# Kernel optimization log

Measured on AMD Instinct MI355X. Metric: run time of the kernel, lower is better.

## Reference

```python
import jax, jax.numpy as jnp
import numpy as np

N_NODES = 8192
N_EDGES = 262144
D_FEAT = 512
NHID = 32
LATENT = 16


def setup_inputs() -> dict:
    key = jax.random.key(0)
    ks = jax.random.split(key, 12)
    inp = {
        "features": jax.random.normal(ks[0], (N_NODES, D_FEAT), dtype=jnp.float32),
        "edge_src": jax.random.randint(ks[1], (N_EDGES,), 0, N_NODES, dtype=jnp.int32),
        "edge_dst": jax.random.randint(ks[2], (N_EDGES,), 0, N_NODES, dtype=jnp.int32),
        "edge_weight": jax.random.uniform(ks[3], (N_EDGES,), dtype=jnp.float32),
        # GCEncoder params (GCNConv: out = A @ (x W) + b)
        "Wg1": jax.random.normal(ks[4], (D_FEAT, NHID), dtype=jnp.float32) / np.sqrt(D_FEAT),
        "bg1": jnp.zeros((NHID,), jnp.float32),
        "Wg2": jax.random.normal(ks[5], (NHID, LATENT), dtype=jnp.float32) / np.sqrt(NHID),
        "bg2": jnp.zeros((LATENT,), jnp.float32),
        # MLP encoder params
        "We1": jax.random.normal(ks[6], (D_FEAT, NHID), dtype=jnp.float32) / np.sqrt(D_FEAT),
        "be1": jnp.zeros((NHID,), jnp.float32),
        "We2": jax.random.normal(ks[7], (NHID, LATENT), dtype=jnp.float32) / np.sqrt(NHID),
        "be2": jnp.zeros((LATENT,), jnp.float32),
        # MLP decoder params (latent -> features)
        "Wd1": jax.random.normal(ks[8], (LATENT, NHID), dtype=jnp.float32) / np.sqrt(LATENT),
        "bd1": jnp.zeros((NHID,), jnp.float32),
        "Wd2": jax.random.normal(ks[9], (NHID, D_FEAT), dtype=jnp.float32) / np.sqrt(NHID),
        "bd2": jnp.zeros((D_FEAT,), jnp.float32),
    }
    return inp


def _gcn_conv(x, W, b, edge_src, edge_dst, edge_weight, n_nodes):
    # transform then sparse aggregate: A @ (x W) + b
    xw = x @ W                                   # [N, out]
    msg = xw[edge_src] * edge_weight[:, None]    # [E, out]
    agg = jax.ops.segment_sum(msg, edge_dst, num_segments=n_nodes)
    return agg + b


def reference(features, edge_src, edge_dst, edge_weight,
              Wg1, bg1, Wg2, bg2, We1, be1, We2, be2, Wd1, bd1, Wd2, bd2):
    n = features.shape[0]
    # GCEncoder (dropout p=0.0)
    h = jax.nn.relu(_gcn_conv(features, Wg1, bg1, edge_src, edge_dst, edge_weight, n))
    za = jax.nn.relu(_gcn_conv(h, Wg2, bg2, edge_src, edge_dst, edge_weight, n))
    # MLP encoder
    zx = jax.nn.relu(jax.nn.relu(features @ We1 + be1) @ We2 + be2)
    # concat latents
    z = jnp.concatenate([za, zx], axis=1)        # [N, 2*latent]
    # inner-product decoder: sigmoid(z z^T)  -> [N, N]
    adj_recon = jax.nn.sigmoid(z @ z.T)
    # feature decoder MLP
    feat_recon = jax.nn.relu(jax.nn.relu(zx @ Wd1 + bd1) @ Wd2 + bd2)
    return adj_recon, feat_recon, z
```

## Files before the change

kernel.cpp:

```cpp
#include <hip/hip_runtime.h>

typedef unsigned short ushort_t;
typedef __attribute__((ext_vector_type(8))) short short8;
typedef __attribute__((ext_vector_type(4))) float floatx4;
typedef __attribute__((ext_vector_type(2))) float floatx2;

#define N_NODES 8192
#define N_EDGES 262144
#define D_FEAT 512
#define NHID 32
#define LATENT 16

#define ADJ_OFF 0
#define FEAT_OFF (8192*8192)
#define Z_OFF (8192*8192 + 8192*512)

static __device__ __forceinline__ ushort_t f2bf(float f) {
    unsigned int u = __float_as_uint(f);
    unsigned int r = u + 0x7fffu + ((u >> 16) & 1u);
    return (ushort_t)(r >> 16);
}

__global__ __launch_bounds__(256) void k_zero(int* __restrict__ counts) {
    int i = blockIdx.x * 256 + threadIdx.x;
    if (i < N_NODES) counts[i] = 0;
}

__global__ __launch_bounds__(256) void k_hist(const int* __restrict__ edst, int* __restrict__ counts) {
    int e = blockIdx.x * 256 + threadIdx.x;
    atomicAdd(&counts[edst[e]], 1);
}

__global__ __launch_bounds__(1024) void k_scan(const int* __restrict__ counts,
                                               int* __restrict__ offs, int* __restrict__ cursor) {
    __shared__ int sdata[1024];
    int t = threadIdx.x;
    int base = t * 8;
    int c[8], local[8];
    int s = 0;
    #pragma unroll
    for (int j = 0; j < 8; j++) { c[j] = counts[base + j]; }
    #pragma unroll
    for (int j = 0; j < 8; j++) { local[j] = s; s += c[j]; }
    sdata[t] = s;
    __syncthreads();
    for (int off = 1; off < 1024; off <<= 1) {
        int v = sdata[t];
        int add = (t >= off) ? sdata[t - off] : 0;
        __syncthreads();
        sdata[t] = v + add;
        __syncthreads();
    }
    int excl = (t == 0) ? 0 : sdata[t - 1];
    #pragma unroll
    for (int j = 0; j < 8; j++) {
        int o = excl + local[j];
        offs[base + j] = o;
        cursor[base + j] = o;
    }
}

__global__ __launch_bounds__(256) void k_scatter(const int* __restrict__ esrc,
                                                 const int* __restrict__ edst,
                                                 const float* __restrict__ ew,
                                                 int* __restrict__ cursor,
                                                 int2* __restrict__ sedge) {
    int e = blockIdx.x * 256 + threadIdx.x;
    int d = edst[e];
    int pos = atomicAdd(&cursor[d], 1);
    sedge[pos] = make_int2(esrc[e], __float_as_int(ew[e]));
}

__global__ __launch_bounds__(256) void k_enc(const float* __restrict__ feat,
                                             const float* __restrict__ Wg1,
                                             const float* __restrict__ We1,
                                             const float* __restrict__ be1,
                                             const float* __restrict__ We2,
                                             const float* __restrict__ be2,
                                             float* __restrict__ xwg,
                                             float* __restrict__ zxf) {
    __shared__ float WL[32][64];
    __shared__ float FL[32][33];
    __shared__ float HE[32][33];
    int tid = threadIdx.x;
    int cr = tid & 15;
    int nr = tid >> 4;
    int m0 = blockIdx.x * 32;
    float acc[2][4] = {};

    for (int kt = 0; kt < 16; kt++) {
        __syncthreads();
        {
            int i = tid;
            #pragma unroll
            for (int j = 0; j < 8; j++, i += 256) {
                int k = i >> 6, c = i & 63;
                int kg = kt * 32 + k;
                WL[k][c] = (c < 32) ? Wg1[kg * 32 + c] : We1[kg * 32 + (c - 32)];
            }
        }
        {
            int n = tid >> 3, q = tid & 7;
            float4 v = *(const float4*)(feat + (m0 + n) * 512 + kt * 32 + q * 4);
            FL[n][q * 4 + 0] = v.x; FL[n][q * 4 + 1] = v.y;
            FL[n][q * 4 + 2] = v.z; FL[n][q * 4 + 3] = v.w;
        }
        __syncthreads();
        #pragma unroll 4
        for (int k = 0; k < 32; k++) {
            float4 w = *(const float4*)&WL[k][cr * 4];
            float f0 = FL[nr * 2 + 0][k];
            float f1 = FL[nr * 2 + 1][k];
            acc[0][0] += f0 * w.x; acc[0][1] += f0 * w.y;
            acc[0][2] += f0 * w.z; acc[0][3] += f0 * w.w;
            acc[1][0] += f1 * w.x; acc[1][1] += f1 * w.y;
            acc[1][2] += f1 * w.z; acc[1][3] += f1 * w.w;
        }
    }
    int cg = cr * 4;
    if (cg < 32) {
        #pragma unroll
        for (int j = 0; j < 2; j++) {
            float4 v = make_float4(acc[j][0], acc[j][1], acc[j][2], acc[j][3]);
            *(float4*)(xwg + (m0 + nr * 2 + j) * 32 + cg) = v;
        }
    } else {
        int hc = cg - 32;
        #pragma unroll
        for (int j = 0; j < 2; j++) {
            #pragma unroll
            for (int t = 0; t < 4; t++) {
                float v = acc[j][t] + be1[hc + t];
                HE[nr * 2 + j][hc + t] = v > 0.f ? v : 0.f;
            }
        }
    }
    __syncthreads();
    int n = tid >> 3, j0 = (tid & 7) * 2;
    float s0 = be2[j0], s1 = be2[j0 + 1];
    #pragma unroll 8
    for (int cc = 0; cc < 32; cc++) {
        float h = HE[n][cc];
        s0 += h * We2[cc * 16 + j0];
        s1 += h * We2[cc * 16 + j0 + 1];
    }
    s0 = s0 > 0.f ? s0 : 0.f;
    s1 = s1 > 0.f ? s1 : 0.f;
    *(float2*)(zxf + (m0 + n) * 16 + j0) = make_float2(s0, s1);
}

__global__ __launch_bounds__(256) void k_agg1(const float* __restrict__ xwg,
                                              const int* __restrict__ offs,
                                              const int* __restrict__ counts,
                                              const int2* __restrict__ sedge,
                                              const float* __restrict__ bg1,
                                              const float* __restrict__ Wg2,
                                              float* __restrict__ hw2) {
    __shared__ float hsh[8][33];
    int ln = threadIdx.x >> 5, c = threadIdx.x & 31;
    int n = blockIdx.x * 8 + ln;
    int st = offs[n], en = st + counts[n];
    float acc = 0.f;
    int i = st;
    for (; i + 4 <= en; i += 4) {
        int2 e0 = sedge[i], e1 = sedge[i + 1], e2 = sedge[i + 2], e3 = sedge[i + 3];
        float s0 = __int_as_float(e0.y) * xwg[e0.x * 32 + c];
        float s1 = __int_as_float(e1.y) * xwg[e1.x * 32 + c];
        float s2 = __int_as_float(e2.y) * xwg[e2.x * 32 + c];
        float s3 = __int_as_float(e3.y) * xwg[e3.x * 32 + c];
        acc += (s0 + s1) + (s2 + s3);
    }
    for (; i < en; i++) {
        int2 e = sedge[i];
        acc += __int_as_float(e.y) * xwg[e.x * 32 + c];
    }
    float h = acc + bg1[c];
    hsh[ln][c] = h > 0.f ? h : 0.f;
    __syncthreads();
    if (threadIdx.x < 128) {
        int l2 = threadIdx.x >> 4, j = threadIdx.x & 15;
        float s2 = 0.f;
        #pragma unroll 8
        for (int cc = 0; cc < 32; cc++) s2 += hsh[l2][cc] * Wg2[cc * 16 + j];
        hw2[(blockIdx.x * 8 + l2) * 16 + j] = s2;
    }
}

__global__ __launch_bounds__(256) void k_agg2(const float* __restrict__ hw2,
                                              const int* __restrict__ offs,
                                              const int* __restrict__ counts,
                                              const int2* __restrict__ sedge,
                                              const float* __restrict__ bg2,
                                              const float* __restrict__ zxf,
                                              ushort_t* __restrict__ zbf,
                                              float* __restrict__ zout) {
    int ln = threadIdx.x >> 4, c = threadIdx.x & 15;
    int n = blockIdx.x * 16 + ln;
    int st = offs[n], en = st + counts[n];
    float acc = 0.f;
    int i = st;
    for (; i + 4 <= en; i += 4) {
        int2 e0 = sedge[i], e1 = sedge[i + 1], e2 = sedge[i + 2], e3 = sedge[i + 3];
        float s0 = __int_as_float(e0.y) * hw2[e0.x * 16 + c];
        float s1 = __int_as_float(e1.y) * hw2[e1.x * 16 + c];
        float s2 = __int_as_float(e2.y) * hw2[e2.x * 16 + c];
        float s3 = __int_as_float(e3.y) * hw2[e3.x * 16 + c];
        acc += (s0 + s1) + (s2 + s3);
    }
    for (; i < en; i++) {
        int2 e = sedge[i];
        acc += __int_as_float(e.y) * hw2[e.x * 16 + c];
    }
    float za = acc + bg2[c];
    za = za > 0.f ? za : 0.f;
    float zx = zxf[n * 16 + c];
    zout[n * 32 + c] = za;
    zout[n * 32 + 16 + c] = zx;
    zbf[n * 32 + c] = f2bf(za);
    zbf[n * 32 + 16 + c] = f2bf(zx);
}

__global__ __launch_bounds__(256) void k_feat(const float* __restrict__ zxf,
                                              const float* __restrict__ Wd1,
                                              const float* __restrict__ bd1,
                                              const float* __restrict__ Wd2,
                                              const float* __restrict__ bd2,
                                              float* __restrict__ outF) {
    __shared__ float ZL[16][17];
    __shared__ float HT[16][33];
    int tid = threadIdx.x;
    int m0 = blockIdx.x * 16;
    {
        int n = tid >> 4, k = tid & 15;
        ZL[n][k] = zxf[(m0 + n) * 16 + k];
    }
    __syncthreads();
    {
        int o = tid * 2;
        int n = o >> 5, c = o & 31;
        float s0 = bd1[c], s1 = bd1[c + 1];
        #pragma unroll
        for (int k = 0; k < 16; k++) {
            float z = ZL[n][k];
            s0 += z * Wd1[k * 32 + c];
            s1 += z * Wd1[k * 32 + c + 1];
        }
        HT[n][c] = s0 > 0.f ? s0 : 0.f;
        HT[n][c + 1] = s1 > 0.f ? s1 : 0.f;
    }
    __syncthreads();
    int c2 = tid * 2;
    floatx2 acc[16];
    #pragma unroll
    for (int n = 0; n < 16; n++) acc[n] = (floatx2){0.f, 0.f};
    for (int k = 0; k < 32; k++) {
        float2 w = *(const float2*)(Wd2 + k * 512 + c2);
        #pragma unroll
        for (int n = 0; n < 16; n++) {
            float t = HT[n][k];
            acc[n].x += t * w.x;
            acc[n].y += t * w.y;
        }
    }
    float b0 = bd2[c2], b1 = bd2[c2 + 1];
    #pragma unroll
    for (int n = 0; n < 16; n++) {
        float s0 = acc[n].x + b0, s1 = acc[n].y + b1;
        s0 = s0 > 0.f ? s0 : 0.f;
        s1 = s1 > 0.f ? s1 : 0.f;
        floatx2 pk = {s0, s1};
        __builtin_nontemporal_store(pk, (floatx2*)(outF + (size_t)(m0 + n) * 512 + c2));
    }
}

__global__ __launch_bounds__(256) void k_adj(const ushort_t* __restrict__ zbf,
                                             float* __restrict__ out) {
    int l = threadIdx.x & 63;
    int wv = threadIdx.x >> 6;
    int strip = blockIdx.x & 15;
    int rt = (blockIdx.x >> 4) * 4 + wv;
    int q = l >> 4, cl = l & 15;
    int m0 = rt * 16, c0 = strip * 512;
    short8 a = *(const short8*)(zbf + (m0 + cl) * 32 + q * 8);
    for (int g = 0; g < 8; g++) {
        int cb = c0 + g * 64;
        short8 b0 = *(const short8*)(zbf + (cb + 4 * cl + 0) * 32 + q * 8);
        short8 b1 = *(const short8*)(zbf + (cb + 4 * cl + 1) * 32 + q * 8);
        short8 b2 = *(const short8*)(zbf + (cb + 4 * cl + 2) * 32 + q * 8);
        short8 b3 = *(const short8*)(zbf + (cb + 4 * cl + 3) * 32 + q * 8);
        floatx4 zv = {0, 0, 0, 0};
        floatx4 a0 = __builtin_amdgcn_mfma_f32_16x16x32_bf16(a, b0, zv, 0, 0, 0);
        floatx4 a1 = __builtin_amdgcn_mfma_f32_16x16x32_bf16(a, b1, zv, 0, 0, 0);
        floatx4 a2 = __builtin_amdgcn_mfma_f32_16x16x32_bf16(a, b2, zv, 0, 0, 0);
        floatx4 a3 = __builtin_amdgcn_mfma_f32_16x16x32_bf16(a, b3, zv, 0, 0, 0);
        #pragma unroll
        for (int r = 0; r < 4; r++) {
            floatx4 v;
            v.x = 1.f / (1.f + __expf(-a0[r]));
            v.y = 1.f / (1.f + __expf(-a1[r]));
            v.z = 1.f / (1.f + __expf(-a2[r]));
            v.w = 1.f / (1.f + __expf(-a3[r]));
            int row = m0 + q * 4 + r;
            __builtin_nontemporal_store(v, (floatx4*)(out + (size_t)row * 8192 + cb + 4 * cl));
        }
    }
}

extern "C" void kernel_launch(void* const* d_in, const int* in_sizes, int n_in,
                              void* d_out, int out_size, void* d_ws, size_t ws_size,
                              hipStream_t stream) {
    const float* feat = (const float*)d_in[0];
    const int* esrc = (const int*)d_in[1];
    const int* edst = (const int*)d_in[2];
    const float* ew = (const float*)d_in[3];
    const float* Wg1 = (const float*)d_in[4];
    const float* bg1 = (const float*)d_in[5];
    const float* Wg2 = (const float*)d_in[6];
    const float* bg2 = (const float*)d_in[7];
    const float* We1 = (const float*)d_in[8];
    const float* be1 = (const float*)d_in[9];
    const float* We2 = (const float*)d_in[10];
    const float* be2 = (const float*)d_in[11];
    const float* Wd1 = (const float*)d_in[12];
    const float* bd1 = (const float*)d_in[13];
    const float* Wd2 = (const float*)d_in[14];
    const float* bd2 = (const float*)d_in[15];
    float* out = (float*)d_out;

    char* ws = (char*)d_ws;
    float* xwg      = (float*)(ws + 0);
    float* zxf      = (float*)(ws + 1048576);
    float* hw2      = (float*)(ws + 1572864);
    ushort_t* zbf   = (ushort_t*)(ws + 2097152);
    int* counts     = (int*)(ws + 2621440);
    int* offs       = (int*)(ws + 2654208);
    int* cursor     = (int*)(ws + 2686976);
    int2* sedge     = (int2*)(ws + 2719744);

    k_zero<<<32, 256, 0, stream>>>(counts);
    k_hist<<<N_EDGES / 256, 256, 0, stream>>>(edst, counts);
    k_scan<<<1, 1024, 0, stream>>>(counts, offs, cursor);
    k_scatter<<<N_EDGES / 256, 256, 0, stream>>>(esrc, edst, ew, cursor, sedge);
    k_enc<<<N_NODES / 32, 256, 0, stream>>>(feat, Wg1, We1, be1, We2, be2, xwg, zxf);
    k_agg1<<<N_NODES / 8, 256, 0, stream>>>(xwg, offs, counts, sedge, bg1, Wg2, hw2);
    k_agg2<<<N_NODES / 16, 256, 0, stream>>>(hw2, offs, counts, sedge, bg2, zxf,
                                             zbf, out + Z_OFF);
    k_feat<<<N_NODES / 16, 256, 0, stream>>>(zxf, Wd1, bd1, Wd2, bd2, out + FEAT_OFF);
    k_adj<<<(N_NODES / 16 / 4) * 16, 256, 0, stream>>>(zbf, out + ADJ_OFF);
}
```

Baseline: 454.7 us.

## Fuse graph build and GCN aggregation into persistent kernel with grid barriers

```diff
diff --git a/kernel.cpp b/kernel.cpp
--- a/kernel.cpp
+++ b/kernel.cpp
@@ -15,60 +15,25 @@
 #define FEAT_OFF (8192*8192)
 #define Z_OFF (8192*8192 + 8192*512)
 
+#define GCN_BLOCKS 512
+
 static __device__ __forceinline__ ushort_t f2bf(float f) {
     unsigned int u = __float_as_uint(f);
     unsigned int r = u + 0x7fffu + ((u >> 16) & 1u);
     return (ushort_t)(r >> 16);
 }
 
-__global__ __launch_bounds__(256) void k_zero(int* __restrict__ counts) {
-    int i = blockIdx.x * 256 + threadIdx.x;
-    if (i < N_NODES) counts[i] = 0;
-}
-
-__global__ __launch_bounds__(256) void k_hist(const int* __restrict__ edst, int* __restrict__ counts) {
-    int e = blockIdx.x * 256 + threadIdx.x;
-    atomicAdd(&counts[edst[e]], 1);
-}
-
-__global__ __launch_bounds__(1024) void k_scan(const int* __restrict__ counts,
-                                               int* __restrict__ offs, int* __restrict__ cursor) {
-    __shared__ int sdata[1024];
-    int t = threadIdx.x;
-    int base = t * 8;
-    int c[8], local[8];
-    int s = 0;
-    #pragma unroll
-    for (int j = 0; j < 8; j++) { c[j] = counts[base + j]; }
-    #pragma unroll
-    for (int j = 0; j < 8; j++) { local[j] = s; s += c[j]; }
-    sdata[t] = s;
+static __device__ __forceinline__ void gbar(int* bar, int target) {
+    __threadfence();
     __syncthreads();
-    for (int off = 1; off < 1024; off <<= 1) {
-        int v = sdata[t];
-        int add = (t >= off) ? sdata[t - off] : 0;
-        __syncthreads();
-        sdata[t] = v + add;
-        __syncthreads();
-    }
-    int excl = (t == 0) ? 0 : sdata[t - 1];
-    #pragma unroll
-    for (int j = 0; j < 8; j++) {
-        int o = excl + local[j];
-        offs[base + j] = o;
-        cursor[base + j] = o;
-    }
-}
-
-__global__ __launch_bounds__(256) void k_scatter(const int* __restrict__ esrc,
-                                                 const int* __restrict__ edst,
-                                                 const float* __restrict__ ew,
-                                                 int* __restrict__ cursor,
-                                                 int2* __restrict__ sedge) {
-    int e = blockIdx.x * 256 + threadIdx.x;
-    int d = edst[e];
-    int pos = atomicAdd(&cursor[d], 1);
-    sedge[pos] = make_int2(esrc[e], __float_as_int(ew[e]));
+    if (threadIdx.x == 0) {
+        __hip_atomic_fetch_add(bar, 1, __ATOMIC_ACQ_REL, __HIP_MEMORY_SCOPE_AGENT);
+        while (__hip_atomic_load(bar, __ATOMIC_ACQUIRE, __HIP_MEMORY_SCOPE_AGENT) < target) {
+            __builtin_amdgcn_s_sleep(8);
+        }
+    }
+    __syncthreads();
+    __threadfence();
 }
 
 __global__ __launch_bounds__(256) void k_enc(const float* __restrict__ feat,
@@ -78,11 +43,17 @@
                                              const float* __restrict__ We2,
                                              const float* __restrict__ be2,
                                              float* __restrict__ xwg,
-                                             float* __restrict__ zxf) {
+                                             float* __restrict__ zxf,
+                                             int* __restrict__ counts,
+                                             int* __restrict__ bar) {
     __shared__ float WL[32][64];
     __shared__ float FL[32][33];
     __shared__ float HE[32][33];
     int tid = threadIdx.x;
+    int gid = blockIdx.x * 256 + tid;
+    if (gid < N_NODES) counts[gid] = 0;
+    if (gid == 0) *bar = 0;
+
     int cr = tid & 15;
     int nr = tid >> 4;
     int m0 = blockIdx.x * 32;
@@ -149,159 +120,212 @@
     *(float2*)(zxf + (m0 + n) * 16 + j0) = make_float2(s0, s1);
 }
 
-__global__ __launch_bounds__(256) void k_agg1(const float* __restrict__ xwg,
-                                              const int* __restrict__ offs,
-                                              const int* __restrict__ counts,
-                                              const int2* __restrict__ sedge,
-                                              const float* __restrict__ bg1,
-                                              const float* __restrict__ Wg2,
-                                              float* __restrict__ hw2) {
-    __shared__ float hsh[8][33];
-    int ln = threadIdx.x >> 5, c = threadIdx.x & 31;
-    int n = blockIdx.x * 8 + ln;
-    int st = offs[n], en = st + counts[n];
-    float acc = 0.f;
-    int i = st;
-    for (; i + 4 <= en; i += 4) {
-        int2 e0 = sedge[i], e1 = sedge[i + 1], e2 = sedge[i + 2], e3 = sedge[i + 3];
-        float s0 = __int_as_float(e0.y) * xwg[e0.x * 32 + c];
-        float s1 = __int_as_float(e1.y) * xwg[e1.x * 32 + c];
-        float s2 = __int_as_float(e2.y) * xwg[e2.x * 32 + c];
-        float s3 = __int_as_float(e3.y) * xwg[e3.x * 32 + c];
-        acc += (s0 + s1) + (s2 + s3);
-    }
-    for (; i < en; i++) {
-        int2 e = sedge[i];
-        acc += __int_as_float(e.y) * xwg[e.x * 32 + c];
-    }
-    float h = acc + bg1[c];
-    hsh[ln][c] = h > 0.f ? h : 0.f;
-    __syncthreads();
-    if (threadIdx.x < 128) {
-        int l2 = threadIdx.x >> 4, j = threadIdx.x & 15;
+__global__ __launch_bounds__(256, 2) void k_gcn(const int* __restrict__ esrc,
+                                                const int* __restrict__ edst,
+                                                const float* __restrict__ ew,
+                                                const float* __restrict__ xwg,
+                                                const float* __restrict__ bg1,
+                                                const float* __restrict__ Wg2,
+                                                const float* __restrict__ bg2,
+                                                const float* __restrict__ zxf,
+                                                int* __restrict__ counts,
+                                                int* __restrict__ offs,
+                                                int* __restrict__ cursor,
+                                                int2* __restrict__ sedge,
+                                                float* __restrict__ hw2,
+                                                ushort_t* __restrict__ zbf,
+                                                float* __restrict__ zout,
+                                                int* __restrict__ bar) {
+    __shared__ int ps[256];
+    __shared__ float hsh[16][33];
+    int tid = threadIdx.x;
+    int b = blockIdx.x;
+
+    int e0 = b * 512;
+    #pragma unroll
+    for (int r = 0; r < 2; r++) {
+        int e = e0 + r * 256 + tid;
+        atomicAdd(&counts[edst[e]], 1);
+    }
+    gbar(bar, GCN_BLOCKS);
+
+    if (b == 0) {
+        int base = tid * 32;
+        int loc[32];
+        int s = 0;
+        #pragma unroll
+        for (int j = 0; j < 32; j++) { loc[j] = s; s += counts[base + j]; }
+        ps[tid] = s;
+        __syncthreads();
+        for (int off = 1; off < 256; off <<= 1) {
+            int v = ps[tid];
+            int a = (tid >= off) ? ps[tid - off] : 0;
+            __syncthreads();
+            ps[tid] = v + a;
+            __syncthreads();
+        }
+        int excl = tid ? ps[tid - 1] : 0;
+        #pragma unroll
+        for (int j = 0; j < 32; j++) {
+            int o = excl + loc[j];
+            offs[base + j] = o;
+            cursor[base + j] = o;
+        }
+    }
+    gbar(bar, 2 * GCN_BLOCKS);
+
+    #pragma unroll
+    for (int r = 0; r < 2; r++) {
+        int e = e0 + r * 256 + tid;
+        int d = edst[e];
+        int pos = atomicAdd(&cursor[d], 1);
+        sedge[pos] = make_int2(esrc[e], __float_as_int(ew[e]));
+    }
+    gbar(bar, 3 * GCN_BLOCKS);
+
+    {
+        int ln = tid >> 5, c = tid & 31;
+        for (int pass = 0; pass < 2; pass++) {
+            int n = b * 16 + pass * 8 + ln;
+            int st = offs[n], en = st + counts[n];
+            float acc = 0.f;
+            int i = st;
+            for (; i + 4 <= en; i += 4) {
+                int2 q0 = sedge[i], q1 = sedge[i + 1], q2 = sedge[i + 2], q3 = sedge[i + 3];
+                float v0 = __int_as_float(q0.y) * xwg[q0.x * 32 + c];
+                float v1 = __int_as_float(q1.y) * xwg[q1.x * 32 + c];
+                float v2 = __int_as_float(q2.y) * xwg[q2.x * 32 + c];
+                float v3 = __int_as_float(q3.y) * xwg[q3.x * 32 + c];
+                acc += (v0 + v1) + (v2 + v3);
+            }
+            for (; i < en; i++) {
+                int2 q = sedge[i];
+                acc += __int_as_float(q.y) * xwg[q.x * 32 + c];
+            }
+            float h = acc + bg1[c];
+            hsh[pass * 8 + ln][c] = h > 0.f ? h : 0.f;
+        }
+        __syncthreads();
+        int n2 = tid >> 4, j = tid & 15;
         float s2 = 0.f;
         #pragma unroll 8
-        for (int cc = 0; cc < 32; cc++) s2 += hsh[l2][cc] * Wg2[cc * 16 + j];
-        hw2[(blockIdx.x * 8 + l2) * 16 + j] = s2;
-    }
-}
-
-__global__ __launch_bounds__(256) void k_agg2(const float* __restrict__ hw2,
-                                              const int* __restrict__ offs,
-                                              const int* __restrict__ counts,
-                                              const int2* __restrict__ sedge,
-                                              const float* __restrict__ bg2,
-                                              const float* __restrict__ zxf,
-                                              ushort_t* __restrict__ zbf,
-                                              float* __restrict__ zout) {
-    int ln = threadIdx.x >> 4, c = threadIdx.x & 15;
-    int n = blockIdx.x * 16 + ln;
-    int st = offs[n], en = st + counts[n];
-    float acc = 0.f;
-    int i = st;
-    for (; i + 4 <= en; i += 4) {
-        int2 e0 = sedge[i], e1 = sedge[i + 1], e2 = sedge[i + 2], e3 = sedge[i + 3];
-        float s0 = __int_as_float(e0.y) * hw2[e0.x * 16 + c];
-        float s1 = __int_as_float(e1.y) * hw2[e1.x * 16 + c];
-        float s2 = __int_as_float(e2.y) * hw2[e2.x * 16 + c];
-        float s3 = __int_as_float(e3.y) * hw2[e3.x * 16 + c];
-        acc += (s0 + s1) + (s2 + s3);
-    }
-    for (; i < en; i++) {
-        int2 e = sedge[i];
-        acc += __int_as_float(e.y) * hw2[e.x * 16 + c];
-    }
-    float za = acc + bg2[c];
-    za = za > 0.f ? za : 0.f;
-    float zx = zxf[n * 16 + c];
-    zout[n * 32 + c] = za;
-    zout[n * 32 + 16 + c] = zx;
-    zbf[n * 32 + c] = f2bf(za);
-    zbf[n * 32 + 16 + c] = f2bf(zx);
-}
-
-__global__ __launch_bounds__(256) void k_feat(const float* __restrict__ zxf,
-                                              const float* __restrict__ Wd1,
-                                              const float* __restrict__ bd1,
-                                              const float* __restrict__ Wd2,
-                                              const float* __restrict__ bd2,
-                                              float* __restrict__ outF) {
+        for (int cc = 0; cc < 32; cc++) s2 += hsh[n2][cc] * Wg2[cc * 16 + j];
+        hw2[(b * 16 + n2) * 16 + j] = s2;
+    }
+    gbar(bar, 4 * GCN_BLOCKS);
+
+    {
+        int ln = tid >> 4, c = tid & 15;
+        int n = b * 16 + ln;
+        int st = offs[n], en = st + counts[n];
+        float acc = 0.f;
+        int i = st;
+        for (; i + 4 <= en; i += 4) {
+            int2 q0 = sedge[i], q1 = sedge[i + 1], q2 = sedge[i + 2], q3 = sedge[i + 3];
+            float v0 = __int_as_float(q0.y) * hw2[q0.x * 16 + c];
+            float v1 = __int_as_float(q1.y) * hw2[q1.x * 16 + c];
+            float v2 = __int_as_float(q2.y) * hw2[q2.x * 16 + c];
+            float v3 = __int_as_float(q3.y) * hw2[q3.x * 16 + c];
+            acc += (v0 + v1) + (v2 + v3);
+        }
+        for (; i < en; i++) {
+            int2 q = sedge[i];
+            acc += __int_as_float(q.y) * hw2[q.x * 16 + c];
+        }
+        float za = acc + bg2[c];
+        za = za > 0.f ? za : 0.f;
+        float zx = zxf[n * 16 + c];
+        zout[n * 32 + c] = za;
+        zout[n * 32 + 16 + c] = zx;
+        zbf[n * 32 + c] = f2bf(za);
+        zbf[n * 32 + 16 + c] = f2bf(zx);
+    }
+}
+
+__global__ __launch_bounds__(256) void k_out(const ushort_t* __restrict__ zbf,
+                                             const float* __restrict__ zxf,
+                                             const float* __restrict__ Wd1,
+                                             const float* __restrict__ bd1,
+                                             const float* __restrict__ Wd2,
+                                             const float* __restrict__ bd2,
+                                             float* __restrict__ out) {
     __shared__ float ZL[16][17];
     __shared__ float HT[16][33];
     int tid = threadIdx.x;
-    int m0 = blockIdx.x * 16;
-    {
-        int n = tid >> 4, k = tid & 15;
-        ZL[n][k] = zxf[(m0 + n) * 16 + k];
-    }
-    __syncthreads();
-    {
-        int o = tid * 2;
-        int n = o >> 5, c = o & 31;
-        float s0 = bd1[c], s1 = bd1[c + 1];
-        #pragma unroll
-        for (int k = 0; k < 16; k++) {
-            float z = ZL[n][k];
-            s0 += z * Wd1[k * 32 + c];
-            s1 += z * Wd1[k * 32 + c + 1];
-        }
-        HT[n][c] = s0 > 0.f ? s0 : 0.f;
-        HT[n][c + 1] = s1 > 0.f ? s1 : 0.f;
-    }
-    __syncthreads();
-    int c2 = tid * 2;
-    floatx2 acc[16];
-    #pragma unroll
-    for (int n = 0; n < 16; n++) acc[n] = (floatx2){0.f, 0.f};
-    for (int k = 0; k < 32; k++) {
-        float2 w = *(const float2*)(Wd2 + k * 512 + c2);
+    if (blockIdx.x < 2048) {
+        float* adj = out + ADJ_OFF;
+        int l = tid & 63;
+        int wv = tid >> 6;
+        int strip = blockIdx.x & 15;
+        int rt = (blockIdx.x >> 4) * 4 + wv;
+        int q = l >> 4, cl = l & 15;
+        int m0 = rt * 16, c0 = strip * 512;
+        short8 a = *(const short8*)(zbf + (m0 + cl) * 32 + q * 8);
+        for (int g = 0; g < 8; g++) {
+            int cb = c0 + g * 64;
+            short8 b0 = *(const short8*)(zbf + (cb + 4 * cl + 0) * 32 + q * 8);
+            short8 b1 = *(const short8*)(zbf + (cb + 4 * cl + 1) * 32 + q * 8);
+            short8 b2 = *(const short8*)(zbf + (cb + 4 * cl + 2) * 32 + q * 8);
+            short8 b3 = *(const short8*)(zbf + (cb + 4 * cl + 3) * 32 + q * 8);
+            floatx4 zv = {0, 0, 0, 0};
+            floatx4 a0 = __builtin_amdgcn_mfma_f32_16x16x32_bf16(a, b0, zv, 0, 0, 0);
+            floatx4 a1 = __builtin_amdgcn_mfma_f32_16x16x32_bf16(a, b1, zv, 0, 0, 0);
+            floatx4 a2 = __builtin_amdgcn_mfma_f32_16x16x32_bf16(a, b2, zv, 0, 0, 0);
+            floatx4 a3 = __builtin_amdgcn_mfma_f32_16x16x32_bf16(a, b3, zv, 0, 0, 0);
+            #pragma unroll
+            for (int r = 0; r < 4; r++) {
+                floatx4 v;
+                v.x = 1.f / (1.f + __expf(-a0[r]));
+                v.y = 1.f / (1.f + __expf(-a1[r]));
+                v.z = 1.f / (1.f + __expf(-a2[r]));
+                v.w = 1.f / (1.f + __expf(-a3[r]));
+                int row = m0 + q * 4 + r;
+                __builtin_nontemporal_store(v, (floatx4*)(adj + (size_t)row * 8192 + cb + 4 * cl));
+            }
+        }
+    } else {
+        float* outF = out + FEAT_OFF;
+        int m0 = (blockIdx.x - 2048) * 16;
+        {
+            int n = tid >> 4, k = tid & 15;
+            ZL[n][k] = zxf[(m0 + n) * 16 + k];
+        }
+        __syncthreads();
+        {
+            int o = tid * 2;
+            int n = o >> 5, c = o & 31;
+            float s0 = bd1[c], s1 = bd1[c + 1];
+            #pragma unroll
+            for (int k = 0; k < 16; k++) {
+                float z = ZL[n][k];
+                s0 += z * Wd1[k * 32 + c];
+                s1 += z * Wd1[k * 32 + c + 1];
+            }
+            HT[n][c] = s0 > 0.f ? s0 : 0.f;
+            HT[n][c + 1] = s1 > 0.f ? s1 : 0.f;
+        }
+        __syncthreads();
+        int c2 = tid * 2;
+        floatx2 acc[16];
+        #pragma unroll
+        for (int n = 0; n < 16; n++) acc[n] = (floatx2){0.f, 0.f};
+        for (int k = 0; k < 32; k++) {
+            float2 w = *(const float2*)(Wd2 + k * 512 + c2);
+            #pragma unroll
+            for (int n = 0; n < 16; n++) {
+                float t = HT[n][k];
+                acc[n].x += t * w.x;
+                acc[n].y += t * w.y;
+            }
+        }
+        float b0 = bd2[c2], b1 = bd2[c2 + 1];
         #pragma unroll
         for (int n = 0; n < 16; n++) {
-            float t = HT[n][k];
-            acc[n].x += t * w.x;
-            acc[n].y += t * w.y;
-        }
-    }
-    float b0 = bd2[c2], b1 = bd2[c2 + 1];
-    #pragma unroll
-    for (int n = 0; n < 16; n++) {
-        float s0 = acc[n].x + b0, s1 = acc[n].y + b1;
-        s0 = s0 > 0.f ? s0 : 0.f;
-        s1 = s1 > 0.f ? s1 : 0.f;
-        floatx2 pk = {s0, s1};
-        __builtin_nontemporal_store(pk, (floatx2*)(outF + (size_t)(m0 + n) * 512 + c2));
-    }
-}
-
-__global__ __launch_bounds__(256) void k_adj(const ushort_t* __restrict__ zbf,
-                                             float* __restrict__ out) {
-    int l = threadIdx.x & 63;
-    int wv = threadIdx.x >> 6;
-    int strip = blockIdx.x & 15;
-    int rt = (blockIdx.x >> 4) * 4 + wv;
-    int q = l >> 4, cl = l & 15;
-    int m0 = rt * 16, c0 = strip * 512;
-    short8 a = *(const short8*)(zbf + (m0 + cl) * 32 + q * 8);
-    for (int g = 0; g < 8; g++) {
-        int cb = c0 + g * 64;
-        short8 b0 = *(const short8*)(zbf + (cb + 4 * cl + 0) * 32 + q * 8);
-        short8 b1 = *(const short8*)(zbf + (cb + 4 * cl + 1) * 32 + q * 8);
-        short8 b2 = *(const short8*)(zbf + (cb + 4 * cl + 2) * 32 + q * 8);
-        short8 b3 = *(const short8*)(zbf + (cb + 4 * cl + 3) * 32 + q * 8);
-        floatx4 zv = {0, 0, 0, 0};
-        floatx4 a0 = __builtin_amdgcn_mfma_f32_16x16x32_bf16(a, b0, zv, 0, 0, 0);
-        floatx4 a1 = __builtin_amdgcn_mfma_f32_16x16x32_bf16(a, b1, zv, 0, 0, 0);
-        floatx4 a2 = __builtin_amdgcn_mfma_f32_16x16x32_bf16(a, b2, zv, 0, 0, 0);
-        floatx4 a3 = __builtin_amdgcn_mfma_f32_16x16x32_bf16(a, b3, zv, 0, 0, 0);
-        #pragma unroll
-        for (int r = 0; r < 4; r++) {
-            floatx4 v;
-            v.x = 1.f / (1.f + __expf(-a0[r]));
-            v.y = 1.f / (1.f + __expf(-a1[r]));
-            v.z = 1.f / (1.f + __expf(-a2[r]));
-            v.w = 1.f / (1.f + __expf(-a3[r]));
-            int row = m0 + q * 4 + r;
-            __builtin_nontemporal_store(v, (floatx4*)(out + (size_t)row * 8192 + cb + 4 * cl));
+            float s0 = acc[n].x + b0, s1 = acc[n].y + b1;
+            s0 = s0 > 0.f ? s0 : 0.f;
+            s1 = s1 > 0.f ? s1 : 0.f;
+            floatx2 pk = {s0, s1};
+            __builtin_nontemporal_store(pk, (floatx2*)(outF + (size_t)(m0 + n) * 512 + c2));
         }
     }
 }
@@ -335,16 +359,13 @@
     int* counts     = (int*)(ws + 2621440);
     int* offs       = (int*)(ws + 2654208);
     int* cursor     = (int*)(ws + 2686976);
-    int2* sedge     = (int2*)(ws + 2719744);
-
-    k_zero<<<32, 256, 0, stream>>>(counts);
-    k_hist<<<N_EDGES / 256, 256, 0, stream>>>(edst, counts);
-    k_scan<<<1, 1024, 0, stream>>>(counts, offs, cursor);
-    k_scatter<<<N_EDGES / 256, 256, 0, stream>>>(esrc, edst, ew, cursor, sedge);
-    k_enc<<<N_NODES / 32, 256, 0, stream>>>(feat, Wg1, We1, be1, We2, be2, xwg, zxf);
-    k_agg1<<<N_NODES / 8, 256, 0, stream>>>(xwg, offs, counts, sedge, bg1, Wg2, hw2);
-    k_agg2<<<N_NODES / 16, 256, 0, stream>>>(hw2, offs, counts, sedge, bg2, zxf,
-                                             zbf, out + Z_OFF);
-    k_feat<<<N_NODES / 16, 256, 0, stream>>>(zxf, Wd1, bd1, Wd2, bd2, out + FEAT_OFF);
-    k_adj<<<(N_NODES / 16 / 4) * 16, 256, 0, stream>>>(zbf, out + ADJ_OFF);
-}
+    int* bar        = (int*)(ws + 2719744);
+    int2* sedge     = (int2*)(ws + 2719872);
+
+    k_enc<<<N_NODES / 32, 256, 0, stream>>>(feat, Wg1, We1, be1, We2, be2,
+                                            xwg, zxf, counts, bar);
+    k_gcn<<<GCN_BLOCKS, 256, 0, stream>>>(esrc, edst, ew, xwg, bg1, Wg2, bg2, zxf,
+                                          counts, offs, cursor, sedge, hw2,
+                                          zbf, out + Z_OFF, bar);
+    k_out<<<2048 + 512, 256, 0, stream>>>(zbf, zxf, Wd1, bd1, Wd2, bd2, out);
+}
```

Result: slower. 865.6 us (+90.4%).

## Fuse zeroing into encoder, merge feature and adjacency decoders, use fast sigmoid

Applied to the files above, without the earlier changes.

```diff
diff --git a/kernel.cpp b/kernel.cpp
--- a/kernel.cpp
+++ b/kernel.cpp
@@ -21,9 +21,78 @@
     return (ushort_t)(r >> 16);
 }
 
-__global__ __launch_bounds__(256) void k_zero(int* __restrict__ counts) {
-    int i = blockIdx.x * 256 + threadIdx.x;
-    if (i < N_NODES) counts[i] = 0;
+static __device__ __forceinline__ float fsig(float x) {
+    float e = __builtin_amdgcn_exp2f(x * -1.44269504f);
+    return __builtin_amdgcn_rcpf(1.f + e);
+}
+
+__global__ __launch_bounds__(256) void k_enc(const float* __restrict__ feat,
+                                             const float* __restrict__ Wg1,
+                                             const float* __restrict__ We1,
+                                             const float* __restrict__ be1,
+                                             const float* __restrict__ We2,
+                                             const float* __restrict__ be2,
+                                             float* __restrict__ xwg,
+                                             float* __restrict__ zxf,
+                                             int* __restrict__ counts) {
+    __shared__ float WL[32][64];
+    __shared__ float FL[16][36];
+    __shared__ float HE[16][33];
+    int tid = threadIdx.x;
+    int gid = blockIdx.x * 256 + tid;
+    if (gid < N_NODES) counts[gid] = 0;
+
+    int n = tid >> 4;
+    int cr = tid & 15;
+    int m0 = blockIdx.x * 16;
+    float acc[4] = {};
+
+    for (int kt = 0; kt < 16; kt++) {
+        __syncthreads();
+        {
+            int i = tid;
+            #pragma unroll
+            for (int j = 0; j < 8; j++, i += 256) {
+                int k = i >> 6, c = i & 63;
+                int kg = kt * 32 + k;
+                WL[k][c] = (c < 32) ? Wg1[kg * 32 + c] : We1[kg * 32 + (c - 32)];
+            }
+        }
+        if (tid < 128) {
+            int nn = tid >> 3, q = tid & 7;
+            float4 v = *(const float4*)(feat + (m0 + nn) * 512 + kt * 32 + q * 4);
+            FL[nn][q * 4 + 0] = v.x; FL[nn][q * 4 + 1] = v.y;
+            FL[nn][q * 4 + 2] = v.z; FL[nn][q * 4 + 3] = v.w;
+        }
+        __syncthreads();
+        #pragma unroll 4
+        for (int k = 0; k < 32; k++) {
+            float4 w = *(const float4*)&WL[k][cr * 4];
+            float f0 = FL[n][k];
+            acc[0] += f0 * w.x; acc[1] += f0 * w.y;
+            acc[2] += f0 * w.z; acc[3] += f0 * w.w;
+        }
+    }
+    int cg = cr * 4;
+    if (cg < 32) {
+        float4 v = make_float4(acc[0], acc[1], acc[2], acc[3]);
+        *(float4*)(xwg + (m0 + n) * 32 + cg) = v;
+    } else {
+        int hc = cg - 32;
+        #pragma unroll
+        for (int t = 0; t < 4; t++) {
+            float v = acc[t] + be1[hc + t];
+            HE[n][hc + t] = v > 0.f ? v : 0.f;
+        }
+    }
+    __syncthreads();
+    {
+        int j = cr;
+        float s = be2[j];
+        #pragma unroll 8
+        for (int cc = 0; cc < 32; cc++) s += HE[n][cc] * We2[cc * 16 + j];
+        zxf[(m0 + n) * 16 + j] = s > 0.f ? s : 0.f;
+    }
 }
 
 __global__ __launch_bounds__(256) void k_hist(const int* __restrict__ edst, int* __restrict__ counts) {
@@ -69,84 +138,6 @@
     int d = edst[e];
     int pos = atomicAdd(&cursor[d], 1);
     sedge[pos] = make_int2(esrc[e], __float_as_int(ew[e]));
-}
-
-__global__ __launch_bounds__(256) void k_enc(const float* __restrict__ feat,
-                                             const float* __restrict__ Wg1,
-                                             const float* __restrict__ We1,
-                                             const float* __restrict__ be1,
-                                             const float* __restrict__ We2,
-                                             const float* __restrict__ be2,
-                                             float* __restrict__ xwg,
-                                             float* __restrict__ zxf) {
-    __shared__ float WL[32][64];
-    __shared__ float FL[32][33];
-    __shared__ float HE[32][33];
-    int tid = threadIdx.x;
-    int cr = tid & 15;
-    int nr = tid >> 4;
-    int m0 = blockIdx.x * 32;
-    float acc[2][4] = {};
-
-    for (int kt = 0; kt < 16; kt++) {
-        __syncthreads();
-        {
-            int i = tid;
-            #pragma unroll
-            for (int j = 0; j < 8; j++, i += 256) {
-                int k = i >> 6, c = i & 63;
-                int kg = kt * 32 + k;
-                WL[k][c] = (c < 32) ? Wg1[kg * 32 + c] : We1[kg * 32 + (c - 32)];
-            }
-        }
-        {
-            int n = tid >> 3, q = tid & 7;
-            float4 v = *(const float4*)(feat + (m0 + n) * 512 + kt * 32 + q * 4);
-            FL[n][q * 4 + 0] = v.x; FL[n][q * 4 + 1] = v.y;
-            FL[n][q * 4 + 2] = v.z; FL[n][q * 4 + 3] = v.w;
-        }
-        __syncthreads();
-        #pragma unroll 4
-        for (int k = 0; k < 32; k++) {
-            float4 w = *(const float4*)&WL[k][cr * 4];
-            float f0 = FL[nr * 2 + 0][k];
-            float f1 = FL[nr * 2 + 1][k];
-            acc[0][0] += f0 * w.x; acc[0][1] += f0 * w.y;
-            acc[0][2] += f0 * w.z; acc[0][3] += f0 * w.w;
-            acc[1][0] += f1 * w.x; acc[1][1] += f1 * w.y;
-            acc[1][2] += f1 * w.z; acc[1][3] += f1 * w.w;
-        }
-    }
-    int cg = cr * 4;
-    if (cg < 32) {
-        #pragma unroll
-        for (int j = 0; j < 2; j++) {
-            float4 v = make_float4(acc[j][0], acc[j][1], acc[j][2], acc[j][3]);
-            *(float4*)(xwg + (m0 + nr * 2 + j) * 32 + cg) = v;
-        }
-    } else {
-        int hc = cg - 32;
-        #pragma unroll
-        for (int j = 0; j < 2; j++) {
-            #pragma unroll
-            for (int t = 0; t < 4; t++) {
-                float v = acc[j][t] + be1[hc + t];
-                HE[nr * 2 + j][hc + t] = v > 0.f ? v : 0.f;
-            }
-        }
-    }
-    __syncthreads();
-    int n = tid >> 3, j0 = (tid & 7) * 2;
-    float s0 = be2[j0], s1 = be2[j0 + 1];
-    #pragma unroll 8
-    for (int cc = 0; cc < 32; cc++) {
-        float h = HE[n][cc];
-        s0 += h * We2[cc * 16 + j0];
-        s1 += h * We2[cc * 16 + j0 + 1];
-    }
-    s0 = s0 > 0.f ? s0 : 0.f;
-    s1 = s1 > 0.f ? s1 : 0.f;
-    *(float2*)(zxf + (m0 + n) * 16 + j0) = make_float2(s0, s1);
 }
 
 __global__ __launch_bounds__(256) void k_agg1(const float* __restrict__ xwg,
@@ -220,88 +211,90 @@
     zbf[n * 32 + 16 + c] = f2bf(zx);
 }
 
-__global__ __launch_bounds__(256) void k_feat(const float* __restrict__ zxf,
-                                              const float* __restrict__ Wd1,
-                                              const float* __restrict__ bd1,
-                                              const float* __restrict__ Wd2,
-                                              const float* __restrict__ bd2,
-                                              float* __restrict__ outF) {
+__global__ __launch_bounds__(256) void k_out(const ushort_t* __restrict__ zbf,
+                                             const float* __restrict__ zxf,
+                                             const float* __restrict__ Wd1,
+                                             const float* __restrict__ bd1,
+                                             const float* __restrict__ Wd2,
+                                             const float* __restrict__ bd2,
+                                             float* __restrict__ out) {
     __shared__ float ZL[16][17];
     __shared__ float HT[16][33];
     int tid = threadIdx.x;
-    int m0 = blockIdx.x * 16;
-    {
-        int n = tid >> 4, k = tid & 15;
-        ZL[n][k] = zxf[(m0 + n) * 16 + k];
-    }
-    __syncthreads();
-    {
-        int o = tid * 2;
-        int n = o >> 5, c = o & 31;
-        float s0 = bd1[c], s1 = bd1[c + 1];
+    if (blockIdx.x < 2048) {
+        float* adj = out + ADJ_OFF;
+        int l = tid & 63;
+        int wv = tid >> 6;
+        int strip = blockIdx.x & 15;
+        int rt = (blockIdx.x >> 4) * 4 + wv;
+        int q = l >> 4, cl = l & 15;
+        int m0 = rt * 16, c0 = strip * 512;
+        short8 a = *(const short8*)(zbf + (m0 + cl) * 32 + q * 8);
+        for (int g = 0; g < 8; g++) {
+            int cb = c0 + g * 64;
+            short8 b0 = *(const short8*)(zbf + (cb + 4 * cl + 0) * 32 + q * 8);
+            short8 b1 = *(const short8*)(zbf + (cb + 4 * cl + 1) * 32 + q * 8);
+            short8 b2 = *(const short8*)(zbf + (cb + 4 * cl + 2) * 32 + q * 8);
+            short8 b3 = *(const short8*)(zbf + (cb + 4 * cl + 3) * 32 + q * 8);
+            floatx4 zv = {0, 0, 0, 0};
+            floatx4 a0 = __builtin_amdgcn_mfma_f32_16x16x32_bf16(a, b0, zv, 0, 0, 0);
+            floatx4 a1 = __builtin_amdgcn_mfma_f32_16x16x32_bf16(a, b1, zv, 0, 0, 0);
+            floatx4 a2 = __builtin_amdgcn_mfma_f32_16x16x32_bf16(a, b2, zv, 0, 0, 0);
+            floatx4 a3 = __builtin_amdgcn_mfma_f32_16x16x32_bf16(a, b3, zv, 0, 0, 0);
+            #pragma unroll
+            for (int r = 0; r < 4; r++) {
+                floatx4 v;
+                v.x = fsig(a0[r]);
+                v.y = fsig(a1[r]);
+                v.z = fsig(a2[r]);
+                v.w = fsig(a3[r]);
+                int row = m0 + q * 4 + r;
+                __builtin_nontemporal_store(v, (floatx4*)(adj + (size_t)row * 8192 + cb + 4 * cl));
+            }
+        }
+    } else {
+        float* outF = out + FEAT_OFF;
+        int m0 = (blockIdx.x - 2048) * 16;
+        {
+            int n = tid >> 4, k = tid & 15;
+            ZL[n][k] = zxf[(m0 + n) * 16 + k];
+        }
+        __syncthreads();
+        {
+            int o = tid * 2;
+            int n = o >> 5, c = o & 31;
+            float s0 = bd1[c], s1 = bd1[c + 1];
+            #pragma unroll
+            for (int k = 0; k < 16; k++) {
+                float z = ZL[n][k];
+                s0 += z * Wd1[k * 32 + c];
+                s1 += z * Wd1[k * 32 + c + 1];
+            }
+            HT[n][c] = s0 > 0.f ? s0 : 0.f;
+            HT[n][c + 1] = s1 > 0.f ? s1 : 0.f;
+        }
+        __syncthreads();
+        int c2 = tid * 2;
+        floatx2 acc[16];
         #pragma unroll
-        for (int k = 0; k < 16; k++) {
-            float z = ZL[n][k];
-            s0 += z * Wd1[k * 32 + c];
-            s1 += z * Wd1[k * 32 + c + 1];
-        }
-        HT[n][c] = s0 > 0.f ? s0 : 0.f;
-        HT[n][c + 1] = s1 > 0.f ? s1 : 0.f;
-    }
-    __syncthreads();
-    int c2 = tid * 2;
-    floatx2 acc[16];
-    #pragma unroll
-    for (int n = 0; n < 16; n++) acc[n] = (floatx2){0.f, 0.f};
-    for (int k = 0; k < 32; k++) {
-        float2 w = *(const float2*)(Wd2 + k * 512 + c2);
+        for (int n = 0; n < 16; n++) acc[n] = (floatx2){0.f, 0.f};
+        for (int k = 0; k < 32; k++) {
+            float2 w = *(const float2*)(Wd2 + k * 512 + c2);
+            #pragma unroll
+            for (int n = 0; n < 16; n++) {
+                float t = HT[n][k];
+                acc[n].x += t * w.x;
+                acc[n].y += t * w.y;
+            }
+        }
+        float b0 = bd2[c2], b1 = bd2[c2 + 1];
         #pragma unroll
         for (int n = 0; n < 16; n++) {
-            float t = HT[n][k];
-            acc[n].x += t * w.x;
-            acc[n].y += t * w.y;
-        }
-    }
-    float b0 = bd2[c2], b1 = bd2[c2 + 1];
-    #pragma unroll
-    for (int n = 0; n < 16; n++) {
-        float s0 = acc[n].x + b0, s1 = acc[n].y + b1;
-        s0 = s0 > 0.f ? s0 : 0.f;
-        s1 = s1 > 0.f ? s1 : 0.f;
-        floatx2 pk = {s0, s1};
-        __builtin_nontemporal_store(pk, (floatx2*)(outF + (size_t)(m0 + n) * 512 + c2));
-    }
-}
-
-__global__ __launch_bounds__(256) void k_adj(const ushort_t* __restrict__ zbf,
-                                             float* __restrict__ out) {
-    int l = threadIdx.x & 63;
-    int wv = threadIdx.x >> 6;
-    int strip = blockIdx.x & 15;
-    int rt = (blockIdx.x >> 4) * 4 + wv;
-    int q = l >> 4, cl = l & 15;
-    int m0 = rt * 16, c0 = strip * 512;
-    short8 a = *(const short8*)(zbf + (m0 + cl) * 32 + q * 8);
-    for (int g = 0; g < 8; g++) {
-        int cb = c0 + g * 64;
-        short8 b0 = *(const short8*)(zbf + (cb + 4 * cl + 0) * 32 + q * 8);
-        short8 b1 = *(const short8*)(zbf + (cb + 4 * cl + 1) * 32 + q * 8);
-        short8 b2 = *(const short8*)(zbf + (cb + 4 * cl + 2) * 32 + q * 8);
-        short8 b3 = *(const short8*)(zbf + (cb + 4 * cl + 3) * 32 + q * 8);
-        floatx4 zv = {0, 0, 0, 0};
-        floatx4 a0 = __builtin_amdgcn_mfma_f32_16x16x32_bf16(a, b0, zv, 0, 0, 0);
-        floatx4 a1 = __builtin_amdgcn_mfma_f32_16x16x32_bf16(a, b1, zv, 0, 0, 0);
-        floatx4 a2 = __builtin_amdgcn_mfma_f32_16x16x32_bf16(a, b2, zv, 0, 0, 0);
-        floatx4 a3 = __builtin_amdgcn_mfma_f32_16x16x32_bf16(a, b3, zv, 0, 0, 0);
-        #pragma unroll
-        for (int r = 0; r < 4; r++) {
-            floatx4 v;
-            v.x = 1.f / (1.f + __expf(-a0[r]));
-            v.y = 1.f / (1.f + __expf(-a1[r]));
-            v.z = 1.f / (1.f + __expf(-a2[r]));
-            v.w = 1.f / (1.f + __expf(-a3[r]));
-            int row = m0 + q * 4 + r;
-            __builtin_nontemporal_store(v, (floatx4*)(out + (size_t)row * 8192 + cb + 4 * cl));
+            float s0 = acc[n].x + b0, s1 = acc[n].y + b1;
+            s0 = s0 > 0.f ? s0 : 0.f;
+            s1 = s1 > 0.f ? s1 : 0.f;
+            floatx2 pk = {s0, s1};
+            __builtin_nontemporal_store(pk, (floatx2*)(outF + (size_t)(m0 + n) * 512 + c2));
         }
     }
 }
@@ -337,14 +330,13 @@
     int* cursor     = (int*)(ws + 2686976);
     int2* sedge     = (int2*)(ws + 2719744);
 
-    k_zero<<<32, 256, 0, stream>>>(counts);
+    k_enc<<<N_NODES / 16, 256, 0, stream>>>(feat, Wg1, We1, be1, We2, be2,
+                                            xwg, zxf, counts);
     k_hist<<<N_EDGES / 256, 256, 0, stream>>>(edst, counts);
     k_scan<<<1, 1024, 0, stream>>>(counts, offs, cursor);
     k_scatter<<<N_EDGES / 256, 256, 0, stream>>>(esrc, edst, ew, cursor, sedge);
-    k_enc<<<N_NODES / 32, 256, 0, stream>>>(feat, Wg1, We1, be1, We2, be2, xwg, zxf);
     k_agg1<<<N_NODES / 8, 256, 0, stream>>>(xwg, offs, counts, sedge, bg1, Wg2, hw2);
     k_agg2<<<N_NODES / 16, 256, 0, stream>>>(hw2, offs, counts, sedge, bg2, zxf,
                                              zbf, out + Z_OFF);
-    k_feat<<<N_NODES / 16, 256, 0, stream>>>(zxf, Wd1, bd1, Wd2, bd2, out + FEAT_OFF);
-    k_adj<<<(N_NODES / 16 / 4) * 16, 256, 0, stream>>>(zbf, out + ADJ_OFF);
-}
+    k_out<<<2048 + 512, 256, 0, stream>>>(zbf, zxf, Wd1, bd1, Wd2, bd2, out);
+}
```

Measured after the change: 440.8 us. -3.1%, faster.
